# Kernel optimization log

Hardware: AMD Instinct MI355X
Metric: run time of the kernel (lower is better)

Reference implementation:

```python
import jax, jax.numpy as jnp
import numpy as np


def _adder2d(x, w, stride, padding):
    """AdderNet 'convolution': out[b,o,i,j] = -sum_p |patch[b,p,i,j] - w[o,p]|.

    x: [B, C, H, W], w: [O, C, kh, kw]. Patches are extracted in (C, kh, kw)
    channel-major order, matching torch.nn.functional.unfold / w.reshape(O, -1).
    """
    O, C, kh, kw = w.shape
    patches = jax.lax.conv_general_dilated_patches(
        x, (kh, kw), (stride, stride), [(padding, padding), (padding, padding)])
    B, P, Ho, Wo = patches.shape  # P = C*kh*kw
    p = patches.reshape(B, P, Ho * Wo)
    wf = w.reshape(O, P)

    def per_out(wo):  # sequential over small O to avoid a [B,O,P,L] blowup
        return -jnp.sum(jnp.abs(p - wo[None, :, None]), axis=1)  # [B, L]

    out = jax.lax.map(per_out, wf)  # [O, B, L]
    return jnp.transpose(out, (1, 0, 2)).reshape(B, O, Ho, Wo)


def setup_inputs() -> dict:
    key = jax.random.key(0)
    ks = jax.random.split(key, 5)
    x = jax.random.normal(ks[0], (4096, 1, 28, 28), dtype=jnp.float32)
    w1 = jax.random.normal(ks[1], (16, 1, 3, 3), dtype=jnp.float32)
    w2 = jax.random.normal(ks[2], (32, 16, 3, 3), dtype=jnp.float32)
    w3 = jax.random.normal(ks[3], (16, 32, 3, 3), dtype=jnp.float32)
    w4 = jax.random.normal(ks[4], (10, 16, 3, 3), dtype=jnp.float32)
    return {"x": x, "w1": w1, "w2": w2, "w3": w3, "w4": w4}


def reference(x, w1, w2, w3, w4):
    h = x - 0.5
    h = jax.nn.relu((_adder2d(h, w1, 2, 0) + 10.0) / 4.0)   # [B,16,13,13]
    h = jax.nn.relu((_adder2d(h, w2, 2, 1) + 130.0) / 8.0)  # [B,32,7,7]
    h = jax.nn.relu((_adder2d(h, w3, 2, 1) + 280.0) / 16.0)  # [B,16,4,4]
    h = _adder2d(h, w4, 2, 0)                                # [B,10,1,1]
    h = h.reshape(h.shape[0], -1)                            # [B,10]
    return jax.nn.log_softmax(h, axis=1)
```

## Files before the change

### kernel.cpp

```cpp
#include <hip/hip_runtime.h>
#include <math.h>


#if defined(__has_builtin)
#if __has_builtin(__builtin_amdgcn_sad_u16)
#define HAS_SAD 1
#endif
#endif

__device__ __forceinline__ unsigned sadu16(unsigned a, unsigned b, unsigned acc) {
#ifdef HAS_SAD
  return __builtin_amdgcn_sad_u16(a, b, acc);
#else
  int al = (int)(a & 0xFFFFu), ah = (int)(a >> 16);
  int bl = (int)(b & 0xFFFFu), bh = (int)(b >> 16);
  return acc + (unsigned)(al > bl ? al - bl : bl - al)
             + (unsigned)(ah > bh ? ah - bh : bh - ah);
#endif
}

__device__ __forceinline__ unsigned quant(float v) {
  return (unsigned)fmaf(v, 1024.0f, 8192.5f);
}

#define QPAD 0x20002000u

__global__ __launch_bounds__(256, 3) void adder_net_kernel(
    const float* __restrict__ gx,
    const float* __restrict__ gw1,
    const float* __restrict__ gw2,
    const float* __restrict__ gw3,
    const float* __restrict__ gw4,
    float* __restrict__ gout)
{
  __shared__ __align__(16) unsigned s_w[2304];
  __shared__ __align__(16) unsigned s_a1[4800];
  __shared__ __align__(16) unsigned s_a2[3456];
  __shared__ __align__(16) unsigned s_sm[1104];

  const int t = threadIdx.x;
  const int b = blockIdx.x;

  for (int k = t; k < 784; k += 256) {
    int img = (k >= 392) ? 1 : 0;
    int r = k - img * 392;
    int y = r / 14, xw = r - y * 14;
    const float* px = gx + (size_t)(2 * b + img) * 784 + y * 28 + 2 * xw;
    float2 v = *(const float2*)px;
    s_a2[img * 560 + y * 20 + xw] = quant(v.x - 0.5f) | (quant(v.y - 0.5f) << 16);
  }
  for (int k = t; k < 2304; k += 256) {
    int o = k & 31, r = k >> 5;
    int m = r / 9, pk = r - m * 9;
    int base = o * 144 + 2 * m * 9 + pk;
    s_w[k] = quant(gw2[base]) | (quant(gw2[base + 9]) << 16);
  }
  if (t < 96) {
    int pr = t & 1, r = t >> 1;
    int o = r / 3, kh = r - o * 3;
    const float* pw = gw1 + o * 9 + kh * 3;
    s_sm[t] = pr ? quant(pw[2]) : (quant(pw[0]) | (quant(pw[1]) << 16));
  }
  for (int k = t; k < 720; k += 256) {
    int o = k % 10, r = k / 10;
    int m = r / 9, pk = r - m * 9;
    int base = o * 144 + 2 * m * 9 + pk;
    s_sm[96 + k] = quant(gw4[base]) | (quant(gw4[base + 9]) << 16);
  }
  {
    uint4 pad4 = make_uint4(QPAD, QPAD, QPAD, QPAD);
    uint4* p = (uint4*)s_a1;
    for (int k = t; k < 1200; k += 256) p[k] = pad4;
  }
  __syncthreads();

  if (t < 208) {
    const int img = t & 1;
    const int op  = (t >> 1) & 7;
    const int i   = t >> 4;
    unsigned acc0[13], acc1[13];
#pragma unroll
    for (int j = 0; j < 13; ++j) { acc0[j] = 0u; acc1[j] = 0u; }
    const unsigned* w1a = s_sm + (2 * op) * 6;
    const unsigned* w1b = s_sm + (2 * op + 1) * 6;
#pragma unroll
    for (int kh = 0; kh < 3; ++kh) {
      const unsigned* row = s_a2 + img * 560 + (2 * i + kh) * 20;
      uint4 v0 = *(const uint4*)(row);
      uint4 v1 = *(const uint4*)(row + 4);
      uint4 v2 = *(const uint4*)(row + 8);
      uint2 v3 = *(const uint2*)(row + 12);
      unsigned r[14] = {v0.x, v0.y, v0.z, v0.w, v1.x, v1.y, v1.z, v1.w,
                        v2.x, v2.y, v2.z, v2.w, v3.x, v3.y};
      const unsigned wa01 = w1a[kh * 2], wa2 = w1a[kh * 2 + 1];
      const unsigned wb01 = w1b[kh * 2], wb2 = w1b[kh * 2 + 1];
#pragma unroll
      for (int j = 0; j < 13; ++j) {
        unsigned mw = r[j + 1] & 0xFFFFu;
        acc0[j] = sadu16(r[j], wa01, acc0[j]);
        acc0[j] = sadu16(mw, wa2, acc0[j]);
        acc1[j] = sadu16(r[j], wb01, acc1[j]);
        acc1[j] = sadu16(mw, wb2, acc1[j]);
      }
    }
    unsigned* dst = s_a1 + op * 600 + img * 300 + (i + 1) * 20 + 1;
#pragma unroll
    for (int j = 0; j < 13; ++j) {
      float f0 = fmaxf(fmaf((float)acc0[j], -1.0f / 4096.0f, 2.5f), 0.0f);
      float f1 = fmaxf(fmaf((float)acc1[j], -1.0f / 4096.0f, 2.5f), 0.0f);
      dst[j] = quant(f0) | (quant(f1) << 16);
    }
  }
  __syncthreads();

  for (int k = t; k < 1024; k += 256) {
    int plane = k >> 5, c = k & 31;
    int y, x;
    if (c < 9)       { y = 0; x = c; }
    else if (c < 18) { y = 8; x = c - 9; }
    else if (c < 25) { y = c - 17; x = 0; }
    else             { y = c - 24; x = 8; }
    s_a2[plane * 108 + y * 12 + x] = QPAD;
  }
  if (t < 224) {
    const int img = t & 1;
    const int op  = (t >> 1) & 15;
    const int i   = t >> 5;
    unsigned acc0[7], acc1[7];
#pragma unroll
    for (int j = 0; j < 7; ++j) { acc0[j] = 0u; acc1[j] = 0u; }
#pragma unroll
    for (int m = 0; m < 8; ++m) {
#pragma unroll
      for (int kh = 0; kh < 3; ++kh) {
        const unsigned* row = s_a1 + m * 600 + img * 300 + (2 * i + kh) * 20;
        uint4 v0 = *(const uint4*)(row);
        uint4 v1 = *(const uint4*)(row + 4);
        uint4 v2 = *(const uint4*)(row + 8);
        uint4 v3 = *(const uint4*)(row + 12);
        unsigned r[16] = {v0.x, v0.y, v0.z, v0.w, v1.x, v1.y, v1.z, v1.w,
                          v2.x, v2.y, v2.z, v2.w, v3.x, v3.y, v3.z, v3.w};
        const unsigned* wp = s_w + (m * 3 + kh) * 96 + 2 * op;
        uint2 W0 = *(const uint2*)(wp);
        uint2 W1 = *(const uint2*)(wp + 32);
        uint2 W2 = *(const uint2*)(wp + 64);
#pragma unroll
        for (int j = 0; j < 7; ++j) {
          acc0[j] = sadu16(r[2 * j],     W0.x, acc0[j]);
          acc0[j] = sadu16(r[2 * j + 1], W1.x, acc0[j]);
          acc0[j] = sadu16(r[2 * j + 2], W2.x, acc0[j]);
          acc1[j] = sadu16(r[2 * j],     W0.y, acc1[j]);
          acc1[j] = sadu16(r[2 * j + 1], W1.y, acc1[j]);
          acc1[j] = sadu16(r[2 * j + 2], W2.y, acc1[j]);
        }
      }
    }
    unsigned* dst = s_a2 + ((img * 16 + op) * 9 + i + 1) * 12 + 1;
#pragma unroll
    for (int j = 0; j < 7; ++j) {
      float f0 = fmaxf(fmaf((float)acc0[j], -1.0f / 8192.0f, 16.25f), 0.0f);
      float f1 = fmaxf(fmaf((float)acc1[j], -1.0f / 8192.0f, 16.25f), 0.0f);
      dst[j] = quant(f0) | (quant(f1) << 16);
    }
  }
  __syncthreads();

  for (int k = t; k < 2304; k += 256) {
    int o = k & 15, r = k >> 4;
    int m2 = r / 9, pk = r - m2 * 9;
    int base = o * 288 + 2 * m2 * 9 + pk;
    s_w[k] = quant(gw3[base]) | (quant(gw3[base + 9]) << 16);
  }
  __syncthreads();

  {
    const int img = t & 1;
    const int op  = (t >> 1) & 7;
    const int i   = (t >> 4) & 3;
    const int j   = t >> 6;
    unsigned acc0 = 0u, acc1 = 0u;
#pragma unroll
    for (int m2 = 0; m2 < 16; ++m2) {
#pragma unroll
      for (int kh = 0; kh < 3; ++kh) {
        const unsigned* row = s_a2 + ((img * 16 + m2) * 9 + 2 * i + kh) * 12 + 2 * j;
        uint2 A01 = *(const uint2*)row;
        unsigned A2w = row[2];
        const unsigned* wp = s_w + (m2 * 3 + kh) * 48 + 2 * op;
        uint2 K0 = *(const uint2*)(wp);
        uint2 K1 = *(const uint2*)(wp + 16);
        uint2 K2 = *(const uint2*)(wp + 32);
        acc0 = sadu16(A01.x, K0.x, acc0);
        acc0 = sadu16(A01.y, K1.x, acc0);
        acc0 = sadu16(A2w,  K2.x, acc0);
        acc1 = sadu16(A01.x, K0.y, acc1);
        acc1 = sadu16(A01.y, K1.y, acc1);
        acc1 = sadu16(A2w,  K2.y, acc1);
      }
    }
    float f0 = fmaxf(fmaf((float)acc0, -1.0f / 16384.0f, 17.5f), 0.0f);
    float f1 = fmaxf(fmaf((float)acc1, -1.0f / 16384.0f, 17.5f), 0.0f);
    s_sm[816 + ((img * 8 + op) * 4 + i) * 4 + j] = quant(f0) | (quant(f1) << 16);
  }
  __syncthreads();

  if (t < 160) {
    int o = t % 10, g = t / 10;
    int img = g & 1, m = g >> 1;
    const unsigned* a3 = s_sm + 816 + (img * 8 + m) * 16;
    const unsigned* w4 = s_sm + 96 + m * 90;
    unsigned acc = 0u;
#pragma unroll
    for (int kh = 0; kh < 3; ++kh)
#pragma unroll
      for (int kw = 0; kw < 3; ++kw)
        acc = sadu16(a3[kh * 4 + kw], w4[(kh * 3 + kw) * 10 + o], acc);
    s_a1[t] = acc;
  }
  __syncthreads();
  if (t < 20) {
    int o = t % 10, img = t / 10;
    unsigned s = 0u;
#pragma unroll
    for (int m = 0; m < 8; ++m) s += s_a1[(m * 2 + img) * 10 + o];
    ((float*)s_sm)[1072 + img * 10 + o] = -(float)s * (1.0f / 1024.0f);
  }
  __syncthreads();
  if (t < 20) {
    int o = t % 10, img = t / 10;
    const float* lg = (const float*)s_sm + 1072 + img * 10;
    float mx = lg[0];
#pragma unroll
    for (int k = 1; k < 10; ++k) mx = fmaxf(mx, lg[k]);
    float sum = 0.0f;
#pragma unroll
    for (int k = 0; k < 10; ++k) sum += __expf(lg[k] - mx);
    gout[(size_t)(2 * b + img) * 10 + o] = lg[o] - mx - __logf(sum);
  }
}

extern "C" void kernel_launch(void* const* d_in, const int* in_sizes, int n_in,
                              void* d_out, int out_size, void* d_ws, size_t ws_size,
                              hipStream_t stream) {
  const float* x  = (const float*)d_in[0];
  const float* w1 = (const float*)d_in[1];
  const float* w2 = (const float*)d_in[2];
  const float* w3 = (const float*)d_in[3];
  const float* w4 = (const float*)d_in[4];
  float* out = (float*)d_out;
  adder_net_kernel<<<2048, 256, 0, stream>>>(x, w1, w2, w3, w4, out);
}
```

Measured before the change: 122.7 us.

## Register-block layers 2-3 over four outputs and shrink LDS for higher occupancy

```diff
diff --git a/kernel.cpp b/kernel.cpp
--- a/kernel.cpp
+++ b/kernel.cpp
@@ -25,7 +25,7 @@
 
 #define QPAD 0x20002000u
 
-__global__ __launch_bounds__(256, 3) void adder_net_kernel(
+__global__ __launch_bounds__(256, 4) void adder_net_kernel(
     const float* __restrict__ gx,
     const float* __restrict__ gw1,
     const float* __restrict__ gw2,
@@ -35,8 +35,7 @@
 {
   __shared__ __align__(16) unsigned s_w[2304];
   __shared__ __align__(16) unsigned s_a1[4800];
-  __shared__ __align__(16) unsigned s_a2[3456];
-  __shared__ __align__(16) unsigned s_sm[1104];
+  __shared__ __align__(16) unsigned s_a2[2944];
 
   const int t = threadIdx.x;
   const int b = blockIdx.x;
@@ -50,22 +49,17 @@
     s_a2[img * 560 + y * 20 + xw] = quant(v.x - 0.5f) | (quant(v.y - 0.5f) << 16);
   }
   for (int k = t; k < 2304; k += 256) {
-    int o = k & 31, r = k >> 5;
-    int m = r / 9, pk = r - m * 9;
-    int base = o * 144 + 2 * m * 9 + pk;
+    int g = k / 12, r = k - g * 12;
+    int m = g / 24, g2 = g - m * 24, kh = g2 >> 3, q = g2 & 7;
+    int kw = r >> 2, u = r & 3, o = q * 4 + u;
+    int base = o * 144 + 2 * m * 9 + kh * 3 + kw;
     s_w[k] = quant(gw2[base]) | (quant(gw2[base + 9]) << 16);
   }
   if (t < 96) {
-    int pr = t & 1, r = t >> 1;
-    int o = r / 3, kh = r - o * 3;
-    const float* pw = gw1 + o * 9 + kh * 3;
-    s_sm[t] = pr ? quant(pw[2]) : (quant(pw[0]) | (quant(pw[1]) << 16));
-  }
-  for (int k = t; k < 720; k += 256) {
-    int o = k % 10, r = k / 10;
-    int m = r / 9, pk = r - m * 9;
-    int base = o * 144 + 2 * m * 9 + pk;
-    s_sm[96 + k] = quant(gw4[base]) | (quant(gw4[base + 9]) << 16);
+    int op = t / 12, idx = t - op * 12;
+    int ch = idx / 6, w = idx - ch * 6, kh = w >> 1, half = w & 1;
+    const float* pw = gw1 + (op * 2 + ch) * 9 + kh * 3;
+    s_a2[1120 + t] = half ? quant(pw[2]) : (quant(pw[0]) | (quant(pw[1]) << 16));
   }
   {
     uint4 pad4 = make_uint4(QPAD, QPAD, QPAD, QPAD);
@@ -81,19 +75,23 @@
     unsigned acc0[13], acc1[13];
 #pragma unroll
     for (int j = 0; j < 13; ++j) { acc0[j] = 0u; acc1[j] = 0u; }
-    const unsigned* w1a = s_sm + (2 * op) * 6;
-    const unsigned* w1b = s_sm + (2 * op + 1) * 6;
+    const unsigned* Wp = s_a2 + 1120 + op * 12;
+    uint4 Wa = ((const uint4*)Wp)[0];
+    uint4 Wb = ((const uint4*)Wp)[1];
+    uint4 Wc = ((const uint4*)Wp)[2];
+    unsigned wv[12] = {Wa.x, Wa.y, Wa.z, Wa.w, Wb.x, Wb.y, Wb.z, Wb.w,
+                       Wc.x, Wc.y, Wc.z, Wc.w};
 #pragma unroll
     for (int kh = 0; kh < 3; ++kh) {
-      const unsigned* row = s_a2 + img * 560 + (2 * i + kh) * 20;
-      uint4 v0 = *(const uint4*)(row);
-      uint4 v1 = *(const uint4*)(row + 4);
-      uint4 v2 = *(const uint4*)(row + 8);
-      uint2 v3 = *(const uint2*)(row + 12);
+      const unsigned* rp = s_a2 + img * 560 + (2 * i + kh) * 20;
+      uint4 v0 = *(const uint4*)(rp);
+      uint4 v1 = *(const uint4*)(rp + 4);
+      uint4 v2 = *(const uint4*)(rp + 8);
+      uint2 v3 = *(const uint2*)(rp + 12);
       unsigned r[14] = {v0.x, v0.y, v0.z, v0.w, v1.x, v1.y, v1.z, v1.w,
                         v2.x, v2.y, v2.z, v2.w, v3.x, v3.y};
-      const unsigned wa01 = w1a[kh * 2], wa2 = w1a[kh * 2 + 1];
-      const unsigned wb01 = w1b[kh * 2], wb2 = w1b[kh * 2 + 1];
+      const unsigned wa01 = wv[kh * 2], wa2 = wv[kh * 2 + 1];
+      const unsigned wb01 = wv[6 + kh * 2], wb2 = wv[6 + kh * 2 + 1];
 #pragma unroll
       for (int j = 0; j < 13; ++j) {
         unsigned mw = r[j + 1] & 0xFFFFu;
@@ -103,7 +101,7 @@
         acc1[j] = sadu16(mw, wb2, acc1[j]);
       }
     }
-    unsigned* dst = s_a1 + op * 600 + img * 300 + (i + 1) * 20 + 1;
+    unsigned* dst = s_a1 + (op * 2 + img) * 300 + (i + 1) * 20 + 1;
 #pragma unroll
     for (int j = 0; j < 13; ++j) {
       float f0 = fmaxf(fmaf((float)acc0[j], -1.0f / 4096.0f, 2.5f), 0.0f);
@@ -113,122 +111,172 @@
   }
   __syncthreads();
 
-  for (int k = t; k < 1024; k += 256) {
-    int plane = k >> 5, c = k & 31;
-    int y, x;
-    if (c < 9)       { y = 0; x = c; }
-    else if (c < 18) { y = 8; x = c - 9; }
-    else if (c < 25) { y = c - 17; x = 0; }
-    else             { y = c - 24; x = 8; }
-    s_a2[plane * 108 + y * 12 + x] = QPAD;
-  }
-  if (t < 224) {
+  if (t < 112) {
     const int img = t & 1;
-    const int op  = (t >> 1) & 15;
-    const int i   = t >> 5;
-    unsigned acc0[7], acc1[7];
-#pragma unroll
-    for (int j = 0; j < 7; ++j) { acc0[j] = 0u; acc1[j] = 0u; }
-#pragma unroll
+    const int q   = (t >> 1) & 7;
+    const int i   = t >> 4;
+    unsigned acc[4][7];
+#pragma unroll
+    for (int u = 0; u < 4; ++u)
+#pragma unroll
+      for (int j = 0; j < 7; ++j) acc[u][j] = 0u;
     for (int m = 0; m < 8; ++m) {
+      const unsigned* plane = s_a1 + (m * 2 + img) * 300;
+      const unsigned* wg = s_w + m * 288 + q * 12;
 #pragma unroll
       for (int kh = 0; kh < 3; ++kh) {
-        const unsigned* row = s_a1 + m * 600 + img * 300 + (2 * i + kh) * 20;
-        uint4 v0 = *(const uint4*)(row);
-        uint4 v1 = *(const uint4*)(row + 4);
-        uint4 v2 = *(const uint4*)(row + 8);
-        uint4 v3 = *(const uint4*)(row + 12);
+        const unsigned* rp = plane + (2 * i + kh) * 20;
+        uint4 v0 = *(const uint4*)(rp);
+        uint4 v1 = *(const uint4*)(rp + 4);
+        uint4 v2 = *(const uint4*)(rp + 8);
+        uint4 v3 = *(const uint4*)(rp + 12);
         unsigned r[16] = {v0.x, v0.y, v0.z, v0.w, v1.x, v1.y, v1.z, v1.w,
                           v2.x, v2.y, v2.z, v2.w, v3.x, v3.y, v3.z, v3.w};
-        const unsigned* wp = s_w + (m * 3 + kh) * 96 + 2 * op;
-        uint2 W0 = *(const uint2*)(wp);
-        uint2 W1 = *(const uint2*)(wp + 32);
-        uint2 W2 = *(const uint2*)(wp + 64);
+        uint4 W0 = *(const uint4*)(wg + kh * 96);
+        uint4 W1 = *(const uint4*)(wg + kh * 96 + 4);
+        uint4 W2 = *(const uint4*)(wg + kh * 96 + 8);
 #pragma unroll
         for (int j = 0; j < 7; ++j) {
-          acc0[j] = sadu16(r[2 * j],     W0.x, acc0[j]);
-          acc0[j] = sadu16(r[2 * j + 1], W1.x, acc0[j]);
-          acc0[j] = sadu16(r[2 * j + 2], W2.x, acc0[j]);
-          acc1[j] = sadu16(r[2 * j],     W0.y, acc1[j]);
-          acc1[j] = sadu16(r[2 * j + 1], W1.y, acc1[j]);
-          acc1[j] = sadu16(r[2 * j + 2], W2.y, acc1[j]);
+          acc[0][j] = sadu16(r[2 * j],     W0.x, acc[0][j]);
+          acc[0][j] = sadu16(r[2 * j + 1], W1.x, acc[0][j]);
+          acc[0][j] = sadu16(r[2 * j + 2], W2.x, acc[0][j]);
+          acc[1][j] = sadu16(r[2 * j],     W0.y, acc[1][j]);
+          acc[1][j] = sadu16(r[2 * j + 1], W1.y, acc[1][j]);
+          acc[1][j] = sadu16(r[2 * j + 2], W2.y, acc[1][j]);
+          acc[2][j] = sadu16(r[2 * j],     W0.z, acc[2][j]);
+          acc[2][j] = sadu16(r[2 * j + 1], W1.z, acc[2][j]);
+          acc[2][j] = sadu16(r[2 * j + 2], W2.z, acc[2][j]);
+          acc[3][j] = sadu16(r[2 * j],     W0.w, acc[3][j]);
+          acc[3][j] = sadu16(r[2 * j + 1], W1.w, acc[3][j]);
+          acc[3][j] = sadu16(r[2 * j + 2], W2.w, acc[3][j]);
         }
       }
     }
-    unsigned* dst = s_a2 + ((img * 16 + op) * 9 + i + 1) * 12 + 1;
+    unsigned* d0 = s_a2 + (img * 16 + 2 * q) * 92 + (i + 1) * 10 + 1;
 #pragma unroll
     for (int j = 0; j < 7; ++j) {
-      float f0 = fmaxf(fmaf((float)acc0[j], -1.0f / 8192.0f, 16.25f), 0.0f);
-      float f1 = fmaxf(fmaf((float)acc1[j], -1.0f / 8192.0f, 16.25f), 0.0f);
-      dst[j] = quant(f0) | (quant(f1) << 16);
+      float f0 = fmaxf(fmaf((float)acc[0][j], -1.0f / 8192.0f, 16.25f), 0.0f);
+      float f1 = fmaxf(fmaf((float)acc[1][j], -1.0f / 8192.0f, 16.25f), 0.0f);
+      float f2 = fmaxf(fmaf((float)acc[2][j], -1.0f / 8192.0f, 16.25f), 0.0f);
+      float f3 = fmaxf(fmaf((float)acc[3][j], -1.0f / 8192.0f, 16.25f), 0.0f);
+      d0[j]      = quant(f0) | (quant(f1) << 16);
+      d0[92 + j] = quant(f2) | (quant(f3) << 16);
+    }
+  } else {
+    for (int k = t - 112; k < 1024; k += 144) {
+      int plane = k >> 5, c = k & 31;
+      int y, x;
+      if (c < 9)       { y = 0; x = c; }
+      else if (c < 18) { y = 8; x = c - 9; }
+      else if (c < 25) { y = c - 17; x = 0; }
+      else             { y = c - 24; x = 8; }
+      s_a2[plane * 92 + y * 10 + x] = QPAD;
     }
   }
   __syncthreads();
 
   for (int k = t; k < 2304; k += 256) {
-    int o = k & 15, r = k >> 4;
-    int m2 = r / 9, pk = r - m2 * 9;
-    int base = o * 288 + 2 * m2 * 9 + pk;
+    int g = k / 12, r = k - g * 12;
+    int m2 = g / 12, g2 = g - m2 * 12, kh = g2 >> 2, q = g2 & 3;
+    int kw = r >> 2, u = r & 3, o = q * 4 + u;
+    int base = o * 288 + 2 * m2 * 9 + kh * 3 + kw;
     s_w[k] = quant(gw3[base]) | (quant(gw3[base + 9]) << 16);
   }
+  for (int k = t; k < 720; k += 256) {
+    int o = k % 10, r = k / 10, m = r / 9, pk = r - m * 9;
+    int base = o * 144 + 2 * m * 9 + pk;
+    s_a1[k] = quant(gw4[base]) | (quant(gw4[base + 9]) << 16);
+  }
+  __syncthreads();
+
+  if (t < 128) {
+    const int img = t & 1;
+    const int q   = (t >> 1) & 3;
+    const int i   = (t >> 3) & 3;
+    const int mg  = t >> 5;
+    unsigned acc[4][4];
+#pragma unroll
+    for (int u = 0; u < 4; ++u)
+#pragma unroll
+      for (int j = 0; j < 4; ++j) acc[u][j] = 0u;
+#pragma unroll
+    for (int mm = 0; mm < 4; ++mm) {
+      const int m2 = mg * 4 + mm;
+      const unsigned* plane = s_a2 + (img * 16 + m2) * 92;
+      const unsigned* wg = s_w + m2 * 144 + q * 12;
+#pragma unroll
+      for (int kh = 0; kh < 3; ++kh) {
+        const unsigned* rp = plane + (2 * i + kh) * 10;
+        uint2 a0 = *(const uint2*)(rp);
+        uint2 a1 = *(const uint2*)(rp + 2);
+        uint2 a2 = *(const uint2*)(rp + 4);
+        uint2 a3 = *(const uint2*)(rp + 6);
+        unsigned a8 = rp[8];
+        unsigned r9[9] = {a0.x, a0.y, a1.x, a1.y, a2.x, a2.y, a3.x, a3.y, a8};
+        uint4 W0 = *(const uint4*)(wg + kh * 48);
+        uint4 W1 = *(const uint4*)(wg + kh * 48 + 4);
+        uint4 W2 = *(const uint4*)(wg + kh * 48 + 8);
+#pragma unroll
+        for (int j = 0; j < 4; ++j) {
+          acc[0][j] = sadu16(r9[2 * j],     W0.x, acc[0][j]);
+          acc[0][j] = sadu16(r9[2 * j + 1], W1.x, acc[0][j]);
+          acc[0][j] = sadu16(r9[2 * j + 2], W2.x, acc[0][j]);
+          acc[1][j] = sadu16(r9[2 * j],     W0.y, acc[1][j]);
+          acc[1][j] = sadu16(r9[2 * j + 1], W1.y, acc[1][j]);
+          acc[1][j] = sadu16(r9[2 * j + 2], W2.y, acc[1][j]);
+          acc[2][j] = sadu16(r9[2 * j],     W0.z, acc[2][j]);
+          acc[2][j] = sadu16(r9[2 * j + 1], W1.z, acc[2][j]);
+          acc[2][j] = sadu16(r9[2 * j + 2], W2.z, acc[2][j]);
+          acc[3][j] = sadu16(r9[2 * j],     W0.w, acc[3][j]);
+          acc[3][j] = sadu16(r9[2 * j + 1], W1.w, acc[3][j]);
+          acc[3][j] = sadu16(r9[2 * j + 2], W2.w, acc[3][j]);
+        }
+      }
+    }
+    unsigned* pp = s_a1 + 720 + mg * 512 + (img * 16 + q * 4) * 16 + i * 4;
+#pragma unroll
+    for (int u = 0; u < 4; ++u)
+      *(uint4*)(pp + u * 16) = make_uint4(acc[u][0], acc[u][1], acc[u][2], acc[u][3]);
+  }
   __syncthreads();
 
   {
-    const int img = t & 1;
-    const int op  = (t >> 1) & 7;
-    const int i   = (t >> 4) & 3;
-    const int j   = t >> 6;
-    unsigned acc0 = 0u, acc1 = 0u;
-#pragma unroll
-    for (int m2 = 0; m2 < 16; ++m2) {
-#pragma unroll
-      for (int kh = 0; kh < 3; ++kh) {
-        const unsigned* row = s_a2 + ((img * 16 + m2) * 9 + 2 * i + kh) * 12 + 2 * j;
-        uint2 A01 = *(const uint2*)row;
-        unsigned A2w = row[2];
-        const unsigned* wp = s_w + (m2 * 3 + kh) * 48 + 2 * op;
-        uint2 K0 = *(const uint2*)(wp);
-        uint2 K1 = *(const uint2*)(wp + 16);
-        uint2 K2 = *(const uint2*)(wp + 32);
-        acc0 = sadu16(A01.x, K0.x, acc0);
-        acc0 = sadu16(A01.y, K1.x, acc0);
-        acc0 = sadu16(A2w,  K2.x, acc0);
-        acc1 = sadu16(A01.x, K0.y, acc1);
-        acc1 = sadu16(A01.y, K1.y, acc1);
-        acc1 = sadu16(A2w,  K2.y, acc1);
-      }
-    }
-    float f0 = fmaxf(fmaf((float)acc0, -1.0f / 16384.0f, 17.5f), 0.0f);
-    float f1 = fmaxf(fmaf((float)acc1, -1.0f / 16384.0f, 17.5f), 0.0f);
-    s_sm[816 + ((img * 8 + op) * 4 + i) * 4 + j] = quant(f0) | (quant(f1) << 16);
+    int w = t;
+    int img = w >> 7, m = (w >> 4) & 7, pos = w & 15;
+    int f0 = img * 256 + m * 32 + pos;
+    const unsigned* P = s_a1 + 720;
+    unsigned s0 = P[f0] + P[512 + f0] + P[1024 + f0] + P[1536 + f0];
+    unsigned s1 = P[f0 + 16] + P[512 + f0 + 16] + P[1024 + f0 + 16] + P[1536 + f0 + 16];
+    float f0f = fmaxf(fmaf((float)s0, -1.0f / 16384.0f, 17.5f), 0.0f);
+    float f1f = fmaxf(fmaf((float)s1, -1.0f / 16384.0f, 17.5f), 0.0f);
+    s_a1[2768 + w] = quant(f0f) | (quant(f1f) << 16);
   }
   __syncthreads();
 
   if (t < 160) {
-    int o = t % 10, g = t / 10;
-    int img = g & 1, m = g >> 1;
-    const unsigned* a3 = s_sm + 816 + (img * 8 + m) * 16;
-    const unsigned* w4 = s_sm + 96 + m * 90;
+    int o = t % 10, g = t / 10, img = g & 1, m = g >> 1;
+    const unsigned* a3 = s_a1 + 2768 + (img * 8 + m) * 16;
+    const unsigned* w4 = s_a1 + m * 90;
     unsigned acc = 0u;
 #pragma unroll
     for (int kh = 0; kh < 3; ++kh)
 #pragma unroll
       for (int kw = 0; kw < 3; ++kw)
         acc = sadu16(a3[kh * 4 + kw], w4[(kh * 3 + kw) * 10 + o], acc);
-    s_a1[t] = acc;
+    s_a1[3040 + t] = acc;
   }
   __syncthreads();
   if (t < 20) {
     int o = t % 10, img = t / 10;
     unsigned s = 0u;
 #pragma unroll
-    for (int m = 0; m < 8; ++m) s += s_a1[(m * 2 + img) * 10 + o];
-    ((float*)s_sm)[1072 + img * 10 + o] = -(float)s * (1.0f / 1024.0f);
+    for (int m = 0; m < 8; ++m) s += s_a1[3040 + (m * 2 + img) * 10 + o];
+    ((float*)s_a1)[3200 + img * 10 + o] = -(float)s * (1.0f / 1024.0f);
   }
   __syncthreads();
   if (t < 20) {
     int o = t % 10, img = t / 10;
-    const float* lg = (const float*)s_sm + 1072 + img * 10;
+    const float* lg = (const float*)s_a1 + 3200 + img * 10;
     float mx = lg[0];
 #pragma unroll
     for (int k = 1; k < 10; ++k) mx = fmaxf(mx, lg[k]);
```

Result: no change. 120.5 us (-1.8%).
